# Kernel tuning notes

Hardware: AMD Instinct MI355X
Metric: run time of the kernel (lower is better)

Reference implementation:

```python
import jax, jax.numpy as jnp
import numpy as np

N_NODES = 100000
N_EDGES = 1600000
IN_CH = 128
HID = 128
BN_EPS = 1e-5


def setup_inputs() -> dict:
    key = jax.random.key(0)
    ks = jax.random.split(key, 8)
    s = 1.0 / np.sqrt(HID)
    return {
        "x": jax.random.normal(ks[0], (N_NODES, IN_CH), dtype=jnp.float32),
        "edge_index": jax.random.randint(ks[1], (2, N_EDGES), 0, N_NODES, dtype=jnp.int64),
        "w1_0": jax.random.normal(ks[2], (IN_CH, HID), dtype=jnp.float32) * s,
        "b1_0": jnp.zeros((HID,), dtype=jnp.float32),
        "w2_0": jax.random.normal(ks[3], (HID, HID), dtype=jnp.float32) * s,
        "b2_0": jnp.zeros((HID,), dtype=jnp.float32),
        "gamma_0": jnp.ones((HID,), dtype=jnp.float32),
        "beta_0": jnp.zeros((HID,), dtype=jnp.float32),
        "w1_1": jax.random.normal(ks[4], (HID, HID), dtype=jnp.float32) * s,
        "b1_1": jnp.zeros((HID,), dtype=jnp.float32),
        "w2_1": jax.random.normal(ks[5], (HID, HID), dtype=jnp.float32) * s,
        "b2_1": jnp.zeros((HID,), dtype=jnp.float32),
        "gamma_1": jnp.ones((HID,), dtype=jnp.float32),
        "beta_1": jnp.zeros((HID,), dtype=jnp.float32),
    }


def _gin_layer(x, src, dst, w1, b1, w2, b2, gamma, beta):
    n = x.shape[0]
    # neighbor sum aggregation: scatter-add of source features into destinations
    agg = jax.ops.segment_sum(x[src], dst, num_segments=n)
    h = x + agg  # GINConv with eps = 0: (1 + eps) * x + sum_j x_j
    h = jax.nn.relu(h @ w1 + b1) @ w2 + b2  # 2-layer MLP
    # BatchNorm1d (training mode): batch mean, biased variance
    mean = jnp.mean(h, axis=0)
    var = jnp.mean(jnp.square(h - mean), axis=0)
    h = (h - mean) * jax.lax.rsqrt(var + BN_EPS) * gamma + beta
    return jax.nn.relu(h)


def reference(x, edge_index, w1_0, b1_0, w2_0, b2_0, gamma_0, beta_0,
              w1_1, b1_1, w2_1, b2_1, gamma_1, beta_1):
    src, dst = edge_index[0], edge_index[1]
    h = _gin_layer(x, src, dst, w1_0, b1_0, w2_0, b2_0, gamma_0, beta_0)
    h = _gin_layer(h, src, dst, w1_1, b1_1, w2_1, b2_1, gamma_1, beta_1)
    return h
```

## Files before the change

### kernel.cpp

```cpp
#include <hip/hip_runtime.h>
#include <stdint.h>

#define BN_EPS 1e-5f
#define CHUNK 4096

typedef __attribute__((ext_vector_type(8))) short s16x8;
typedef __attribute__((ext_vector_type(16))) float f32x16;
typedef __attribute__((ext_vector_type(4))) unsigned short u16x4;
typedef unsigned short ushort_t;
typedef _Float16 f16;
typedef __attribute__((ext_vector_type(4))) _Float16 f16x4;

__device__ __forceinline__ ushort_t f2bf(float x) {
    uint32_t u = __float_as_uint(x);
    u += 0x7fff + ((u >> 16) & 1);
    return (ushort_t)(u >> 16);
}
__device__ __forceinline__ float bf2f(ushort_t h) {
    return __uint_as_float(((uint32_t)h) << 16);
}

__global__ void k_wprep(const float* __restrict__ w0, const float* __restrict__ w1,
                        const float* __restrict__ w2, const float* __restrict__ w3,
                        ushort_t* __restrict__ wpl) {
    int mat = blockIdx.x >> 6;
    const float* w = (mat == 0) ? w0 : (mat == 1) ? w1 : (mat == 2) ? w2 : w3;
    int e = ((blockIdx.x & 63) << 8) + threadIdx.x;
    int k = e >> 7, col = e & 127;
    float v = w[e];
    ushort_t h = f2bf(v);
    ushort_t l = f2bf(v - bf2f(h));
    ushort_t* base = wpl + (size_t)mat * 32768;
    base[col * 128 + k] = h;
    base[16384 + col * 128 + k] = l;
}

__global__ void k_x0(const float* __restrict__ in, f16* __restrict__ out, int n4) {
    int i = blockIdx.x * blockDim.x + threadIdx.x;
    int st = gridDim.x * blockDim.x;
    for (; i < n4; i += st) {
        float4 v = ((const float4*)in)[i];
        f16x4 h;
        h[0] = (f16)v.x; h[1] = (f16)v.y; h[2] = (f16)v.z; h[3] = (f16)v.w;
        ((f16x4*)out)[i] = h;
    }
}

__global__ __launch_bounds__(256) void k_x1(const float* __restrict__ h2, const float* __restrict__ stats,
                                            const float* __restrict__ gamma, const float* __restrict__ beta,
                                            float invN, f16* __restrict__ out, int n4) {
    __shared__ float sc[128], sh[128];
    int t = threadIdx.x;
    if (t < 128) {
        float mean = stats[t] * invN;
        float var = stats[128 + t] * invN - mean * mean;
        float s = gamma[t] * rsqrtf(var + BN_EPS);
        sc[t] = s; sh[t] = beta[t] - mean * s;
    }
    __syncthreads();
    int i = blockIdx.x * 256 + t, st = gridDim.x * 256;
    for (; i < n4; i += st) {
        float4 v = ((const float4*)h2)[i];
        int c = (i << 2) & 127;
        f16x4 h;
        h[0] = (f16)fmaxf(v.x * sc[c + 0] + sh[c + 0], 0.f);
        h[1] = (f16)fmaxf(v.y * sc[c + 1] + sh[c + 1], 0.f);
        h[2] = (f16)fmaxf(v.z * sc[c + 2] + sh[c + 2], 0.f);
        h[3] = (f16)fmaxf(v.w * sc[c + 3] + sh[c + 3], 0.f);
        ((f16x4*)out)[i] = h;
    }
}

__global__ __launch_bounds__(256) void k_bin(const int* __restrict__ src, const int* __restrict__ dst,
                                             int E, int NBUK, int CAP,
                                             int* __restrict__ gcursor, uint32_t* __restrict__ binned) {
    __shared__ int hist[128], excl[128], gbase[128], hA[128], hB[128];
    __shared__ uint32_t pbuf[CHUNK];
    __shared__ unsigned char bbuf[CHUNK];
    int t = threadIdx.x;
    int base = blockIdx.x * CHUNK;
    int cnt = E - base; if (cnt > CHUNK) cnt = CHUNK;

    uint32_t pk[16]; int bk[16]; int loc[16];
    if (t < 128) hist[t] = 0;
    __syncthreads();
#pragma unroll
    for (int k = 0; k < 16; ++k) {
        int j = t + (k << 8);
        bk[k] = -1;
        if (j < cnt) {
            int s = src[base + j], d = dst[base + j];
            bk[k] = d >> 10;
            pk[k] = ((uint32_t)s << 10) | (uint32_t)(d & 1023);
            loc[k] = atomicAdd(&hist[bk[k]], 1);
        }
    }
    __syncthreads();
    if (t < 128) hA[t] = (t < NBUK) ? hist[t] : 0;
    __syncthreads();
    {
        int cb = 0;
        int* bufs[2] = {hA, hB};
        for (int off = 1; off < 128; off <<= 1) {
            int* A = bufs[cb]; int* B = bufs[cb ^ 1];
            if (t < 128) B[t] = A[t] + ((t >= off) ? A[t - off] : 0);
            __syncthreads();
            cb ^= 1;
        }
        if (t < 128) excl[t] = bufs[cb][t] - ((t < NBUK) ? hist[t] : 0);
    }
    if (t < NBUK && hist[t] > 0) gbase[t] = atomicAdd(&gcursor[t], hist[t]);
    __syncthreads();
#pragma unroll
    for (int k = 0; k < 16; ++k) {
        if (bk[k] >= 0) {
            int slot = excl[bk[k]] + loc[k];
            pbuf[slot] = pk[k];
            bbuf[slot] = (unsigned char)bk[k];
        }
    }
    __syncthreads();
    for (int j = t; j < cnt; j += 256) {
        int b = bbuf[j];
        int pos = gbase[b] + (j - excl[b]);
        if (pos < CAP) binned[(size_t)b * CAP + pos] = pbuf[j];
    }
}

__global__ void k_bucketscan(const int* __restrict__ gcursor, int NBUK,
                             int* __restrict__ bucketBase, int* __restrict__ rowstart,
                             int N, int E) {
    __shared__ int hA[128], hB[128];
    int t = threadIdx.x;
    int v = (t < NBUK) ? gcursor[t] : 0;
    hA[t] = v;
    __syncthreads();
    int cb = 0;
    int* bufs[2] = {hA, hB};
    for (int off = 1; off < 128; off <<= 1) {
        int* A = bufs[cb]; int* B = bufs[cb ^ 1];
        B[t] = A[t] + ((t >= off) ? A[t - off] : 0);
        __syncthreads();
        cb ^= 1;
    }
    if (t < NBUK) bucketBase[t] = bufs[cb][t] - v;
    if (t == 0) rowstart[N] = E;
}

__global__ __launch_bounds__(1024) void k_bucketcsr(const uint32_t* __restrict__ binned,
                                                    const int* __restrict__ gcursor,
                                                    const int* __restrict__ bucketBase,
                                                    int CAP, int N,
                                                    int* __restrict__ rowstart, int* __restrict__ csr) {
    __shared__ int deg[1024], sA[1024], sB[1024], cur[1024];
    int b = blockIdx.x, t = threadIdx.x;
    int cnt = gcursor[b]; if (cnt > CAP) cnt = CAP;
    int gb = bucketBase[b];
    int nodeBase = b << 10;
    int nloc = N - nodeBase; if (nloc > 1024) nloc = 1024;
    const uint32_t* eb = binned + (size_t)b * CAP;

    deg[t] = 0;
    __syncthreads();
    for (int j = t; j < cnt; j += 1024) atomicAdd(&deg[eb[j] & 1023], 1);
    __syncthreads();
    sA[t] = deg[t];
    __syncthreads();
    int cb2 = 0;
    int* bufs[2] = {sA, sB};
    for (int off = 1; off < 1024; off <<= 1) {
        int* A = bufs[cb2]; int* B = bufs[cb2 ^ 1];
        B[t] = A[t] + ((t >= off) ? A[t - off] : 0);
        __syncthreads();
        cb2 ^= 1;
    }
    int ex = bufs[cb2][t] - deg[t];
    cur[t] = ex;
    if (t < nloc) rowstart[nodeBase + t] = gb + ex;
    __syncthreads();
    for (int j = t; j < cnt; j += 1024) {
        uint32_t e = eb[j];
        int p = atomicAdd(&cur[e & 1023], 1);
        csr[gb + p] = (int)(e >> 10);
    }
}

__global__ __launch_bounds__(256) void k_agg(const f16* __restrict__ plane, int N,
                                             const int* __restrict__ rowstart, const int* __restrict__ csr,
                                             ushort_t* __restrict__ out_hi, ushort_t* __restrict__ out_lo) {
    int node = (int)((blockIdx.x * (size_t)blockDim.x + threadIdx.x) >> 6);
    int lane = threadIdx.x & 63;
    int half = lane >> 5, li = lane & 31, ch4 = li << 2;
    if (node >= N) return;

    float ax = 0.f, ay = 0.f, az = 0.f, aw = 0.f;
    if (half == 0) {
        f16x4 sv = *(const f16x4*)(plane + (size_t)node * 128 + ch4);
        ax = (float)sv[0]; ay = (float)sv[1]; az = (float)sv[2]; aw = (float)sv[3];
    }

    int s0 = rowstart[node], s1 = rowstart[node + 1];
    for (int base2 = s0; base2 < s1; base2 += 64) {
        int m = s1 - base2; if (m > 64) m = 64;
        int idx = (lane < m) ? csr[base2 + lane] : 0;
        for (int j = 0; j < m; j += 8) {
            int r0 = __shfl(idx, j + half, 64);
            int r1 = __shfl(idx, j + 2 + half, 64);
            int r2 = __shfl(idx, j + 4 + half, 64);
            int r3 = __shfl(idx, j + 6 + half, 64);
            f16x4 u0 = *(const f16x4*)(plane + (size_t)r0 * 128 + ch4);
            f16x4 u1 = *(const f16x4*)(plane + (size_t)r1 * 128 + ch4);
            f16x4 u2 = *(const f16x4*)(plane + (size_t)r2 * 128 + ch4);
            f16x4 u3 = *(const f16x4*)(plane + (size_t)r3 * 128 + ch4);
            if (j + half < m)     { ax += (float)u0[0]; ay += (float)u0[1]; az += (float)u0[2]; aw += (float)u0[3]; }
            if (j + 2 + half < m) { ax += (float)u1[0]; ay += (float)u1[1]; az += (float)u1[2]; aw += (float)u1[3]; }
            if (j + 4 + half < m) { ax += (float)u2[0]; ay += (float)u2[1]; az += (float)u2[2]; aw += (float)u2[3]; }
            if (j + 6 + half < m) { ax += (float)u3[0]; ay += (float)u3[1]; az += (float)u3[2]; aw += (float)u3[3]; }
        }
    }
    ax += __shfl(ax, lane ^ 32, 64);
    ay += __shfl(ay, lane ^ 32, 64);
    az += __shfl(az, lane ^ 32, 64);
    aw += __shfl(aw, lane ^ 32, 64);
    if (half == 0) {
        u16x4 hi, lo;
        ushort_t h;
        h = f2bf(ax); hi[0] = h; lo[0] = f2bf(ax - bf2f(h));
        h = f2bf(ay); hi[1] = h; lo[1] = f2bf(ay - bf2f(h));
        h = f2bf(az); hi[2] = h; lo[2] = f2bf(az - bf2f(h));
        h = f2bf(aw); hi[3] = h; lo[3] = f2bf(aw - bf2f(h));
        size_t o = (size_t)node * 128 + ch4;
        *(u16x4*)(out_hi + o) = hi;
        *(u16x4*)(out_lo + o) = lo;
    }
}

__global__ __launch_bounds__(256) void k_mlp(const ushort_t* __restrict__ a_hi, const ushort_t* __restrict__ a_lo,
                                             const ushort_t* __restrict__ w1pl, const ushort_t* __restrict__ w2pl,
                                             const float* __restrict__ bias1, const float* __restrict__ bias2,
                                             float* __restrict__ h2, float* __restrict__ stats,
                                             int M, int ntiles) {
    __shared__ ushort_t lds_a[2][8192];
    __shared__ ushort_t lds_h1[8192];
    int tid = threadIdx.x;
    int lane = tid & 63;
    int wv = tid >> 6;
    int li = lane & 31, half = lane >> 5;
    int col = (wv << 5) + li;
    int khalf = half << 3;
    int rsw = li & 15;

    auto stage_a = [&](int m0, ushort_t* buf) {
        int w = tid >> 6, l = tid & 63;
#pragma unroll
        for (int i = 0; i < 4; ++i) {
            int u = w + (i << 2);
            int ob = (u << 10) + (l << 4);
            int plane = ob >> 13;
            int r = (ob >> 8) & 31;
            int csw = (ob >> 4) & 15;
            int c = csw ^ (r & 15);
            const ushort_t* g = (plane ? a_lo : a_hi) + (((size_t)(m0 + r)) << 7) + (c << 3);
            __builtin_amdgcn_global_load_lds(g, buf + (u << 9), 16, 0, 0);
        }
    };

    s16x8 b1h[8], b1l[8];
#pragma unroll
    for (int ks = 0; ks < 8; ++ks) {
        b1h[ks] = *(const s16x8*)(w1pl + (size_t)col * 128 + ks * 16 + khalf);
        b1l[ks] = *(const s16x8*)(w1pl + 16384 + (size_t)col * 128 + ks * 16 + khalf);
    }
    float b1v = bias1[col], b2v = bias2[col];
    float ssum = 0.f, ssq = 0.f;

    int cur = 0;
    stage_a(blockIdx.x << 5, lds_a[0]);
    asm volatile("s_waitcnt vmcnt(0)" ::: "memory");
    __builtin_amdgcn_sched_barrier(0);
    __builtin_amdgcn_s_barrier();

    for (int ti = blockIdx.x; ti < ntiles; ti += gridDim.x) {
        int m0 = ti << 5;
        int tn = ti + (int)gridDim.x;
        if (tn < ntiles) stage_a(tn << 5, lds_a[cur ^ 1]);

        const ushort_t* A = lds_a[cur];
        f32x16 acc = {}, acc2 = {};
#pragma unroll
        for (int ks = 0; ks < 8; ++ks) {
            int csw = ((ks << 1) + half) ^ rsw;
            s16x8 ah = *(const s16x8*)(A + (li << 7) + (csw << 3));
            s16x8 al = *(const s16x8*)(A + 4096 + (li << 7) + (csw << 3));
            acc  = __builtin_amdgcn_mfma_f32_32x32x16_bf16(ah, b1h[ks], acc, 0, 0, 0);
            acc2 = __builtin_amdgcn_mfma_f32_32x32x16_bf16(ah, b1l[ks], acc2, 0, 0, 0);
            acc2 = __builtin_amdgcn_mfma_f32_32x32x16_bf16(al, b1h[ks], acc2, 0, 0, 0);
        }
        int cch = col >> 3, cw = col & 7;
#pragma unroll
        for (int r = 0; r < 16; ++r) {
            int row = (r & 3) + ((r >> 2) << 3) + (half << 2);
            float v = fmaxf(acc[r] + acc2[r] + b1v, 0.f);
            ushort_t hh = f2bf(v);
            ushort_t ll = f2bf(v - bf2f(hh));
            int o = (row << 7) + ((cch ^ (row & 15)) << 3) + cw;
            lds_h1[o] = hh;
            lds_h1[4096 + o] = ll;
        }
        asm volatile("s_waitcnt lgkmcnt(0)" ::: "memory");
        __builtin_amdgcn_sched_barrier(0);
        __builtin_amdgcn_s_barrier();

        acc = (f32x16){}; acc2 = (f32x16){};
#pragma unroll
        for (int ks = 0; ks < 8; ++ks) {
            int csw = ((ks << 1) + half) ^ rsw;
            s16x8 ah = *(const s16x8*)(lds_h1 + (li << 7) + (csw << 3));
            s16x8 al = *(const s16x8*)(lds_h1 + 4096 + (li << 7) + (csw << 3));
            int k0 = (ks << 4) + khalf;
            s16x8 b2h = *(const s16x8*)(w2pl + (size_t)col * 128 + k0);
            s16x8 b2l = *(const s16x8*)(w2pl + 16384 + (size_t)col * 128 + k0);
            acc  = __builtin_amdgcn_mfma_f32_32x32x16_bf16(ah, b2h, acc, 0, 0, 0);
            acc2 = __builtin_amdgcn_mfma_f32_32x32x16_bf16(ah, b2l, acc2, 0, 0, 0);
            acc2 = __builtin_amdgcn_mfma_f32_32x32x16_bf16(al, b2h, acc2, 0, 0, 0);
        }
#pragma unroll
        for (int r = 0; r < 16; ++r) {
            int row = m0 + (r & 3) + ((r >> 2) << 3) + (half << 2);
            float v = acc[r] + acc2[r] + b2v;
            h2[(size_t)row * 128 + col] = v;
            ssum += v; ssq += v * v;
        }
        asm volatile("s_waitcnt vmcnt(0) lgkmcnt(0)" ::: "memory");
        __builtin_amdgcn_sched_barrier(0);
        __builtin_amdgcn_s_barrier();
        cur ^= 1;
    }
    ssum += __shfl(ssum, lane ^ 32, 64);
    ssq  += __shfl(ssq,  lane ^ 32, 64);
    if (half == 0) {
        atomicAdd(&stats[col], ssum);
        atomicAdd(&stats[128 + col], ssq);
    }
}

__global__ __launch_bounds__(256) void k_bnapply(const float* __restrict__ h2, const float* __restrict__ stats,
                                                 const float* __restrict__ gamma, const float* __restrict__ beta,
                                                 float invN, float* __restrict__ out, int n4) {
    __shared__ float sc[128], sh[128];
    int t = threadIdx.x;
    if (t < 128) {
        float mean = stats[t] * invN;
        float var = stats[128 + t] * invN - mean * mean;
        float s = gamma[t] * rsqrtf(var + BN_EPS);
        sc[t] = s; sh[t] = beta[t] - mean * s;
    }
    __syncthreads();
    int i = blockIdx.x * 256 + t, st = gridDim.x * 256;
    for (; i < n4; i += st) {
        float4 v = ((const float4*)h2)[i];
        int c = (i << 2) & 127;
        v.x = fmaxf(v.x * sc[c + 0] + sh[c + 0], 0.f);
        v.y = fmaxf(v.y * sc[c + 1] + sh[c + 1], 0.f);
        v.z = fmaxf(v.z * sc[c + 2] + sh[c + 2], 0.f);
        v.w = fmaxf(v.w * sc[c + 3] + sh[c + 3], 0.f);
        ((float4*)out)[i] = v;
    }
}

extern "C" void kernel_launch(void* const* d_in, const int* in_sizes, int n_in,
                              void* d_out, int out_size, void* d_ws, size_t ws_size,
                              hipStream_t stream) {
    const float* x      = (const float*)d_in[0];
    const int*   ei     = (const int*)d_in[1];
    const float* w1_0   = (const float*)d_in[2];
    const float* b1_0   = (const float*)d_in[3];
    const float* w2_0   = (const float*)d_in[4];
    const float* b2_0   = (const float*)d_in[5];
    const float* gamma0 = (const float*)d_in[6];
    const float* beta0  = (const float*)d_in[7];
    const float* w1_1   = (const float*)d_in[8];
    const float* b1_1   = (const float*)d_in[9];
    const float* w2_1   = (const float*)d_in[10];
    const float* b2_1   = (const float*)d_in[11];
    const float* gamma1 = (const float*)d_in[12];
    const float* beta1  = (const float*)d_in[13];

    const int N = in_sizes[0] / 128;
    const int E = in_sizes[1] / 2;
    const int* srcI = ei;
    const int* dstI = ei + E;
    const int NBUK = (N + 1023) >> 10;
    const int CAP  = (((E / NBUK) + 2048) + 255) & ~255;

    char* p = (char*)d_ws;
    auto aup = [](size_t v) { return (v + 255) & ~(size_t)255; };
    ushort_t* a_hi   = (ushort_t*)p; p += aup((size_t)N * 128 * 2);
    ushort_t* a_lo   = (ushort_t*)p; p += aup((size_t)N * 128 * 2);
    float*    h2     = (float*)p;    p += aup((size_t)N * 128 * 4);
    f16*      xh     = (f16*)p;      p += aup((size_t)N * 128 * 2);
    int*      rowstart = (int*)p;    p += aup((size_t)(N + 1) * 4);
    int*      csr    = (int*)p;      p += aup((size_t)E * 4);
    uint32_t* binned = (uint32_t*)p; p += aup((size_t)NBUK * CAP * 4);
    ushort_t* wpl    = (ushort_t*)p; p += aup((size_t)4 * 32768 * 2);
    int*      bucketBase = (int*)p;  p += 512;
    int*      gcursor = (int*)p;
    float*    stats0  = (float*)(p + 512);
    float*    stats1  = stats0 + 256;
    hipMemsetAsync(gcursor, 0, 512 + 2048, stream);

    const int ntiles = (N + 31) / 32;
    const float invN = 1.0f / (float)N;
    float* out = (float*)d_out;

    k_wprep<<<256, 256, 0, stream>>>(w1_0, w2_0, w1_1, w2_1, wpl);
    k_x0<<<2048, 256, 0, stream>>>(x, xh, N * 32);
    k_bin<<<(E + CHUNK - 1) / CHUNK, 256, 0, stream>>>(srcI, dstI, E, NBUK, CAP, gcursor, binned);
    k_bucketscan<<<1, 128, 0, stream>>>(gcursor, NBUK, bucketBase, rowstart, N, E);
    k_bucketcsr<<<NBUK, 1024, 0, stream>>>(binned, gcursor, bucketBase, CAP, N, rowstart, csr);

    int aggBlocks = (N + 3) / 4;
    k_agg<<<aggBlocks, 256, 0, stream>>>(xh, N, rowstart, csr, a_hi, a_lo);
    k_mlp<<<768, 256, 0, stream>>>(a_hi, a_lo, wpl, wpl + 32768, b1_0, b2_0, h2, stats0, N, ntiles);
    k_x1<<<2048, 256, 0, stream>>>(h2, stats0, gamma0, beta0, invN, xh, N * 32);
    k_agg<<<aggBlocks, 256, 0, stream>>>(xh, N, rowstart, csr, a_hi, a_lo);
    k_mlp<<<768, 256, 0, stream>>>(a_hi, a_lo, wpl + 65536, wpl + 98304, b1_1, b2_1, h2, stats1, N, ntiles);
    k_bnapply<<<2048, 256, 0, stream>>>(h2, stats1, gamma1, beta1, invN, out, N * 32);
}
```

Before: 446.4 us.

## Launch one MLP block per 32-row tile and pre-swizzle weights per lane

Replaces the persistent 768-block MLP kernel, which double-buffered A tiles in LDS, with a grid of one block per 32-row tile (3125 blocks). Each block loads its tile once, clamping rows and masking stores at the tail. The weight prep now writes the hi/lo bf16 planes in a per-wave, per-k-step, per-lane fragment order, so every lane's B-fragment load is fully contiguous and coalesced. The cost is that each block reloads the 128x128 W1 fragments into registers, and the stats atomics now run once per tile instead of once per persistent block. Load/compute overlap now comes from block-level occupancy instead of explicit double buffering.

```diff
diff --git a/kernel.cpp b/kernel.cpp
--- a/kernel.cpp
+++ b/kernel.cpp
@@ -30,9 +30,12 @@
     float v = w[e];
     ushort_t h = f2bf(v);
     ushort_t l = f2bf(v - bf2f(h));
+    int wv = col >> 5, ks = k >> 4, hf = (k >> 3) & 1, j = k & 7;
+    int lane = (hf << 5) + (col & 31);
+    int idx = ((((wv << 3) + ks) << 6) + lane) << 3;
     ushort_t* base = wpl + (size_t)mat * 32768;
-    base[col * 128 + k] = h;
-    base[16384 + col * 128 + k] = l;
+    base[idx + j] = h;
+    base[16384 + idx + j] = l;
 }
 
 __global__ void k_x0(const float* __restrict__ in, f16* __restrict__ out, int n4) {
@@ -238,103 +241,90 @@
 __global__ __launch_bounds__(256) void k_mlp(const ushort_t* __restrict__ a_hi, const ushort_t* __restrict__ a_lo,
                                              const ushort_t* __restrict__ w1pl, const ushort_t* __restrict__ w2pl,
                                              const float* __restrict__ bias1, const float* __restrict__ bias2,
-                                             float* __restrict__ h2, float* __restrict__ stats,
-                                             int M, int ntiles) {
-    __shared__ ushort_t lds_a[2][8192];
+                                             float* __restrict__ h2, float* __restrict__ stats, int M) {
+    __shared__ ushort_t lds_a[8192];
     __shared__ ushort_t lds_h1[8192];
     int tid = threadIdx.x;
     int lane = tid & 63;
     int wv = tid >> 6;
     int li = lane & 31, half = lane >> 5;
     int col = (wv << 5) + li;
-    int khalf = half << 3;
     int rsw = li & 15;
-
-    auto stage_a = [&](int m0, ushort_t* buf) {
-        int w = tid >> 6, l = tid & 63;
-#pragma unroll
-        for (int i = 0; i < 4; ++i) {
-            int u = w + (i << 2);
-            int ob = (u << 10) + (l << 4);
-            int plane = ob >> 13;
-            int r = (ob >> 8) & 31;
-            int csw = (ob >> 4) & 15;
-            int c = csw ^ (r & 15);
-            const ushort_t* g = (plane ? a_lo : a_hi) + (((size_t)(m0 + r)) << 7) + (c << 3);
-            __builtin_amdgcn_global_load_lds(g, buf + (u << 9), 16, 0, 0);
-        }
-    };
+    int m0 = blockIdx.x << 5;
+
+#pragma unroll
+    for (int i = 0; i < 4; ++i) {
+        int u = wv + (i << 2);
+        int ob = (u << 10) + (lane << 4);
+        int plane = ob >> 13;
+        int r = (ob >> 8) & 31;
+        int csw = (ob >> 4) & 15;
+        int c = csw ^ (r & 15);
+        int row = m0 + r; if (row >= M) row = M - 1;
+        const ushort_t* g = (plane ? a_lo : a_hi) + (((size_t)row) << 7) + (c << 3);
+        __builtin_amdgcn_global_load_lds(g, lds_a + (u << 9), 16, 0, 0);
+    }
 
     s16x8 b1h[8], b1l[8];
 #pragma unroll
     for (int ks = 0; ks < 8; ++ks) {
-        b1h[ks] = *(const s16x8*)(w1pl + (size_t)col * 128 + ks * 16 + khalf);
-        b1l[ks] = *(const s16x8*)(w1pl + 16384 + (size_t)col * 128 + ks * 16 + khalf);
+        int fo = ((((wv << 3) + ks) << 6) + lane) << 3;
+        b1h[ks] = *(const s16x8*)(w1pl + fo);
+        b1l[ks] = *(const s16x8*)(w1pl + 16384 + fo);
     }
     float b1v = bias1[col], b2v = bias2[col];
-    float ssum = 0.f, ssq = 0.f;
-
-    int cur = 0;
-    stage_a(blockIdx.x << 5, lds_a[0]);
+
     asm volatile("s_waitcnt vmcnt(0)" ::: "memory");
     __builtin_amdgcn_sched_barrier(0);
     __builtin_amdgcn_s_barrier();
 
-    for (int ti = blockIdx.x; ti < ntiles; ti += gridDim.x) {
-        int m0 = ti << 5;
-        int tn = ti + (int)gridDim.x;
-        if (tn < ntiles) stage_a(tn << 5, lds_a[cur ^ 1]);
-
-        const ushort_t* A = lds_a[cur];
-        f32x16 acc = {}, acc2 = {};
-#pragma unroll
-        for (int ks = 0; ks < 8; ++ks) {
-            int csw = ((ks << 1) + half) ^ rsw;
-            s16x8 ah = *(const s16x8*)(A + (li << 7) + (csw << 3));
-            s16x8 al = *(const s16x8*)(A + 4096 + (li << 7) + (csw << 3));
-            acc  = __builtin_amdgcn_mfma_f32_32x32x16_bf16(ah, b1h[ks], acc, 0, 0, 0);
-            acc2 = __builtin_amdgcn_mfma_f32_32x32x16_bf16(ah, b1l[ks], acc2, 0, 0, 0);
-            acc2 = __builtin_amdgcn_mfma_f32_32x32x16_bf16(al, b1h[ks], acc2, 0, 0, 0);
-        }
-        int cch = col >> 3, cw = col & 7;
-#pragma unroll
-        for (int r = 0; r < 16; ++r) {
-            int row = (r & 3) + ((r >> 2) << 3) + (half << 2);
-            float v = fmaxf(acc[r] + acc2[r] + b1v, 0.f);
-            ushort_t hh = f2bf(v);
-            ushort_t ll = f2bf(v - bf2f(hh));
-            int o = (row << 7) + ((cch ^ (row & 15)) << 3) + cw;
-            lds_h1[o] = hh;
-            lds_h1[4096 + o] = ll;
-        }
-        asm volatile("s_waitcnt lgkmcnt(0)" ::: "memory");
-        __builtin_amdgcn_sched_barrier(0);
-        __builtin_amdgcn_s_barrier();
-
-        acc = (f32x16){}; acc2 = (f32x16){};
-#pragma unroll
-        for (int ks = 0; ks < 8; ++ks) {
-            int csw = ((ks << 1) + half) ^ rsw;
-            s16x8 ah = *(const s16x8*)(lds_h1 + (li << 7) + (csw << 3));
-            s16x8 al = *(const s16x8*)(lds_h1 + 4096 + (li << 7) + (csw << 3));
-            int k0 = (ks << 4) + khalf;
-            s16x8 b2h = *(const s16x8*)(w2pl + (size_t)col * 128 + k0);
-            s16x8 b2l = *(const s16x8*)(w2pl + 16384 + (size_t)col * 128 + k0);
-            acc  = __builtin_amdgcn_mfma_f32_32x32x16_bf16(ah, b2h, acc, 0, 0, 0);
-            acc2 = __builtin_amdgcn_mfma_f32_32x32x16_bf16(ah, b2l, acc2, 0, 0, 0);
-            acc2 = __builtin_amdgcn_mfma_f32_32x32x16_bf16(al, b2h, acc2, 0, 0, 0);
-        }
-#pragma unroll
-        for (int r = 0; r < 16; ++r) {
-            int row = m0 + (r & 3) + ((r >> 2) << 3) + (half << 2);
+    f32x16 acc = {}, acc2 = {};
+#pragma unroll
+    for (int ks = 0; ks < 8; ++ks) {
+        int csw = ((ks << 1) + half) ^ rsw;
+        s16x8 ah = *(const s16x8*)(lds_a + (li << 7) + (csw << 3));
+        s16x8 al = *(const s16x8*)(lds_a + 4096 + (li << 7) + (csw << 3));
+        acc  = __builtin_amdgcn_mfma_f32_32x32x16_bf16(ah, b1h[ks], acc, 0, 0, 0);
+        acc2 = __builtin_amdgcn_mfma_f32_32x32x16_bf16(ah, b1l[ks], acc2, 0, 0, 0);
+        acc2 = __builtin_amdgcn_mfma_f32_32x32x16_bf16(al, b1h[ks], acc2, 0, 0, 0);
+    }
+    int cch = col >> 3, cw = col & 7;
+#pragma unroll
+    for (int r = 0; r < 16; ++r) {
+        int row = (r & 3) + ((r >> 2) << 3) + (half << 2);
+        float v = fmaxf(acc[r] + acc2[r] + b1v, 0.f);
+        ushort_t hh = f2bf(v);
+        ushort_t ll = f2bf(v - bf2f(hh));
+        int o = (row << 7) + ((cch ^ (row & 15)) << 3) + cw;
+        lds_h1[o] = hh;
+        lds_h1[4096 + o] = ll;
+    }
+    asm volatile("s_waitcnt lgkmcnt(0)" ::: "memory");
+    __builtin_amdgcn_sched_barrier(0);
+    __builtin_amdgcn_s_barrier();
+
+    acc = (f32x16){}; acc2 = (f32x16){};
+#pragma unroll
+    for (int ks = 0; ks < 8; ++ks) {
+        int csw = ((ks << 1) + half) ^ rsw;
+        s16x8 ah = *(const s16x8*)(lds_h1 + (li << 7) + (csw << 3));
+        s16x8 al = *(const s16x8*)(lds_h1 + 4096 + (li << 7) + (csw << 3));
+        int fo = ((((wv << 3) + ks) << 6) + lane) << 3;
+        s16x8 b2h = *(const s16x8*)(w2pl + fo);
+        s16x8 b2l = *(const s16x8*)(w2pl + 16384 + fo);
+        acc  = __builtin_amdgcn_mfma_f32_32x32x16_bf16(ah, b2h, acc, 0, 0, 0);
+        acc2 = __builtin_amdgcn_mfma_f32_32x32x16_bf16(ah, b2l, acc2, 0, 0, 0);
+        acc2 = __builtin_amdgcn_mfma_f32_32x32x16_bf16(al, b2h, acc2, 0, 0, 0);
+    }
+    float ssum = 0.f, ssq = 0.f;
+#pragma unroll
+    for (int r = 0; r < 16; ++r) {
+        int row = m0 + (r & 3) + ((r >> 2) << 3) + (half << 2);
+        if (row < M) {
             float v = acc[r] + acc2[r] + b2v;
             h2[(size_t)row * 128 + col] = v;
             ssum += v; ssq += v * v;
         }
-        asm volatile("s_waitcnt vmcnt(0) lgkmcnt(0)" ::: "memory");
-        __builtin_amdgcn_sched_barrier(0);
-        __builtin_amdgcn_s_barrier();
-        cur ^= 1;
     }
     ssum += __shfl(ssum, lane ^ 32, 64);
     ssq  += __shfl(ssq,  lane ^ 32, 64);
@@ -421,9 +411,9 @@
 
     int aggBlocks = (N + 3) / 4;
     k_agg<<<aggBlocks, 256, 0, stream>>>(xh, N, rowstart, csr, a_hi, a_lo);
-    k_mlp<<<768, 256, 0, stream>>>(a_hi, a_lo, wpl, wpl + 32768, b1_0, b2_0, h2, stats0, N, ntiles);
+    k_mlp<<<ntiles, 256, 0, stream>>>(a_hi, a_lo, wpl, wpl + 32768, b1_0, b2_0, h2, stats0, N);
     k_x1<<<2048, 256, 0, stream>>>(h2, stats0, gamma0, beta0, invN, xh, N * 32);
     k_agg<<<aggBlocks, 256, 0, stream>>>(xh, N, rowstart, csr, a_hi, a_lo);
-    k_mlp<<<768, 256, 0, stream>>>(a_hi, a_lo, wpl + 65536, wpl + 98304, b1_1, b2_1, h2, stats1, N, ntiles);
+    k_mlp<<<ntiles, 256, 0, stream>>>(a_hi, a_lo, wpl + 65536, wpl + 98304, b1_1, b2_1, h2, stats1, N);
     k_bnapply<<<2048, 256, 0, stream>>>(h2, stats1, gamma1, beta1, invN, out, N * 32);
 }
```

Measured after the change: 500.8 us. 1.12x slower.
